# Optimization experiments

Hardware: AMD Instinct MI355X
Metric: run time of the kernel (lower is better)

The kernel has to match this reference:

```python
import jax, jax.numpy as jnp
import numpy as np

# PSLoss constants (from init_kwargs)
MSE_WEIGHT = 0.5
W_CORR = 1.0
W_VAR = 1.0
W_MEAN = 1.0
K = 3           # k_dominant_freqs
MIN_PATCH = 5   # min_patch_len (max(2, 5))
EPS = 1e-8


def setup_inputs() -> dict:
    key = jax.random.key(0)
    k1, k2 = jax.random.split(key)
    B, T, F = 64, 336, 321
    forecast = jax.random.normal(k1, (B, T, F), dtype=jnp.float32)
    target = jax.random.normal(k2, (B, T, F), dtype=jnp.float32)
    return {"forecast": forecast, "target": target}


def _structural_loss(fc, tg):
    """fc, tg: [N, T] flattened (batch*features) series. Returns (total_loss_sum, patch_count)."""
    N, T = tg.shape
    Mmax = T // MIN_PATCH  # max segments per period (period >= MIN_PATCH)

    # --- Fourier adaptive patching (vectorized over all N series) ---
    amp = jnp.abs(jnp.fft.rfft(tg, axis=-1))[:, 1:]           # drop DC, [N, T//2]
    _, rel = jax.lax.top_k(amp, K)                             # [N, K]
    freq_idx = (rel + 1).astype(jnp.float32)
    p = jnp.floor(T / freq_idx).astype(jnp.int32)              # dominant periods [N, K]
    # dedup periods in topk order (the original 'processed_periods' set)
    eq = p[:, :, None] == p[:, None, :]                        # [N, K, K]
    earlier = jnp.tril(jnp.ones((K, K), dtype=bool), -1)       # j < k
    dup = jnp.any(eq & earlier, axis=-1)
    valid_p = (p >= MIN_PATCH) & ~dup                          # [N, K]

    nseg = T // p                                              # [N, K] (p >= 2 always)
    s_idx = jnp.arange(Mmax, dtype=jnp.int32)
    seg_s = p[:, :, None] * s_idx                              # [N, K, Mmax]
    seg_e = seg_s + p[:, :, None]
    seg_v = (s_idx < nseg[:, :, None]) & valid_p[:, :, None]
    rem_s = nseg * p                                           # remaining tail patch
    rem_v = valid_p & ((T - rem_s) >= MIN_PATCH)

    starts = jnp.concatenate([seg_s.reshape(N, -1), rem_s], axis=-1)
    ends = jnp.concatenate([seg_e.reshape(N, -1), jnp.full_like(rem_s, T)], axis=-1)
    valid = jnp.concatenate([seg_v.reshape(N, -1), rem_v], axis=-1)
    # fallback whole-series patch if no patch survived
    none = ~jnp.any(valid, axis=-1, keepdims=True)
    starts = jnp.concatenate([starts, jnp.zeros((N, 1), jnp.int32)], axis=-1)
    ends = jnp.concatenate([ends, jnp.full((N, 1), T, jnp.int32)], axis=-1)
    valid = jnp.concatenate([valid, none], axis=-1)            # [N, M]

    # --- dedup identical (start, end) patches (original list(set(...))) ---
    SENT = (T + 1) * (T + 1)
    keys = jnp.where(valid, starts * (T + 1) + ends, SENT)
    keys = jnp.sort(keys, axis=-1)
    uniq = jnp.concatenate(
        [jnp.ones((N, 1), dtype=bool), keys[:, 1:] != keys[:, :-1]], axis=-1)
    valid = (keys != SENT) & uniq
    s = jnp.where(valid, keys // (T + 1), 0)                   # safe dummy (0,2) when invalid
    e = jnp.where(valid, keys % (T + 1), 2)

    # --- per-patch stats via inclusive prefix sums ---
    def csum(x):
        return jnp.concatenate([jnp.zeros((N, 1), x.dtype), jnp.cumsum(x, axis=-1)], axis=-1)

    cs_t, cs_f = csum(tg), csum(fc)
    cs_tt, cs_ff, cs_tf = csum(tg * tg), csum(fc * fc), csum(tg * fc)

    def seg_sum(cs):
        return jnp.take_along_axis(cs, e, axis=-1) - jnp.take_along_axis(cs, s, axis=-1)

    n = (e - s).astype(jnp.float32)
    St, Sf = seg_sum(cs_t), seg_sum(cs_f)
    Stt, Sff, Stf = seg_sum(cs_tt), seg_sum(cs_ff), seg_sum(cs_tf)
    mt, mf = St / n, Sf / n
    tvs = jnp.maximum(Stt - n * mt * mt, 0.0)   # sum of squared deviations (target)
    fvs = jnp.maximum(Sff - n * mf * mf, 0.0)
    num = Stf - n * mt * mf
    corr = num / (jnp.sqrt(tvs * fvs) + EPS)
    corr_loss = 1.0 - jnp.abs(corr)
    tvar = tvs / (n - 1.0)                      # torch.var is unbiased
    fvar = fvs / (n - 1.0)
    var_loss = jnp.abs(tvar - fvar) / (tvar + EPS)
    mean_loss = jnp.abs(mt - mf) / (jnp.abs(mt) + EPS)
    patch_loss = W_CORR * corr_loss + W_VAR * var_loss + W_MEAN * mean_loss

    total = jnp.sum(jnp.where(valid, patch_loss, 0.0))
    count = jnp.sum(valid)
    return total, count


def reference(forecast, target):
    B, T, F = forecast.shape
    fc = jnp.transpose(forecast, (0, 2, 1)).reshape(B * F, T)
    tg = jnp.transpose(target, (0, 2, 1)).reshape(B * F, T)
    total, count = _structural_loss(fc, tg)
    avg = jnp.where(count > 0,
                    total / jnp.maximum(count, 1).astype(jnp.float32),
                    jnp.float32(0.0))
    mse = jnp.mean((forecast - target) ** 2)
    return MSE_WEIGHT * mse + (1.0 - MSE_WEIGHT) * avg
```

## Files before the change

kernel.cpp:

```cpp
#include <hip/hip_runtime.h>
#include <hip/hip_bf16.h>

#define TT 336
#define NF 321
#define NB 64
#define NSER (NB * NF)
#define WPB 4
#define KP 352
#define LDA 360
#define SPB 16
#define NPATB (NSER / WPB)
#define TSP (TT + 4)

#define SK(b) ((b) + ((b) >> 5))
#define TBL 348

#define TGX 11
#define TGY 11
#define NMSEP (TGX * TGY * NB)

typedef __attribute__((ext_vector_type(8))) short bf16x8;
typedef __attribute__((ext_vector_type(4))) float f32x4;
typedef unsigned long long ULL;

__device__ __forceinline__ unsigned short f2bf(float v) {
    unsigned x = __float_as_uint(v);
    x += 0x7FFFu + ((x >> 16) & 1u);
    return (unsigned short)(x >> 16);
}

__device__ __forceinline__ void ins3(ULL& a0, ULL& a1, ULL& a2, ULL x) {
    ULL hi = a0 > x ? a0 : x;
    ULL lo = a0 > x ? x : a0;
    a0 = hi;
    ULL hi1 = a1 > lo ? a1 : lo;
    ULL lo1 = a1 > lo ? lo : a1;
    a1 = hi1;
    a2 = a2 > lo1 ? a2 : lo1;
}

__global__ void twiddle_k(unsigned short* __restrict__ Wb) {
    int n = blockIdx.x;
    int f = (n >> 1) + 1;
    int isSin = n & 1;
    for (int k = threadIdx.x; k < KP; k += blockDim.x) {
        float v = 0.0f;
        if (k < TT) {
            int r = (f * k) % TT;
            double ang = 6.283185307179586476925286766559 * (double)r / 336.0;
            v = isSin ? (float)sin(ang) : (float)cos(ang);
        }
        Wb[(size_t)n * KP + k] = f2bf(v);
    }
}

__global__ __launch_bounds__(256) void psd_k(const float* __restrict__ tgO,
                                             const unsigned short* __restrict__ Wb,
                                             uint4* __restrict__ topk) {
    __shared__ __align__(16) unsigned short sA[SPB][LDA];
    __shared__ ULL tk3[4][SPB][3];
    const int tid = threadIdx.x;
    const int serBase = blockIdx.x * SPB;

    {
        int f_l = tid & 15, tch = tid >> 4;
        int ser = serBase + f_l;
        int bb = ser / NF, ff = ser - bb * NF;
        const float* base = tgO + (size_t)bb * TT * NF + ff;
        int t0 = tch * 21;
        float v[21];
#pragma unroll
        for (int i = 0; i < 21; i++) v[i] = base[(size_t)(t0 + i) * NF];
#pragma unroll
        for (int i = 0; i < 21; i++) sA[f_l][t0 + i] = f2bf(v[i]);
    }
    if (tid < SPB * 16) sA[tid >> 4][TT + (tid & 15)] = 0;
    __syncthreads();

    const int wave = tid >> 6, lane = tid & 63;
    const int quad = lane >> 4, c = lane & 15;
    const unsigned short* aRow = &sA[c][quad * 8];
    const int ntStart = wave * 5;
    const int ntEnd = (wave == 3) ? 21 : ntStart + 5;

    ULL t0k[4] = {0, 0, 0, 0}, t1k[4] = {0, 0, 0, 0}, t2k[4] = {0, 0, 0, 0};
    for (int nt = ntStart; nt < ntEnd; nt++) {
        const unsigned short* bRow = Wb + (size_t)(nt * 16 + c) * KP + quad * 8;
        f32x4 acc = (f32x4){0.f, 0.f, 0.f, 0.f};
#pragma unroll
        for (int ks = 0; ks < 11; ks++) {
            bf16x8 a = *(const bf16x8*)(aRow + ks * 32);
            bf16x8 b = *(const bf16x8*)(bRow + ks * 32);
            acc = __builtin_amdgcn_mfma_f32_16x16x32_bf16(a, b, acc, 0, 0, 0);
        }
        int n = nt * 16 + c;
        unsigned fidx = (unsigned)((n >> 1) + 1);
        unsigned ftag = 0xFFFFFFFFu - fidx;
        bool odd = (n & 1) != 0;
#pragma unroll
        for (int r = 0; r < 4; r++) {
            float v = acc[r];
            float p = v * v;
            p += __shfl_xor(p, 1, 64);
            ULL key = odd ? 0ull
                          : (((ULL)__float_as_uint(p) << 32) | (ULL)ftag);
            ins3(t0k[r], t1k[r], t2k[r], key);
        }
    }
#pragma unroll
    for (int m = 2; m <= 8; m <<= 1) {
#pragma unroll
        for (int r = 0; r < 4; r++) {
            ULL b0 = __shfl_xor(t0k[r], m, 64);
            ULL b1 = __shfl_xor(t1k[r], m, 64);
            ULL b2 = __shfl_xor(t2k[r], m, 64);
            ins3(t0k[r], t1k[r], t2k[r], b0);
            ins3(t0k[r], t1k[r], t2k[r], b1);
            ins3(t0k[r], t1k[r], t2k[r], b2);
        }
    }
    if (c == 0) {
#pragma unroll
        for (int r = 0; r < 4; r++) {
            int s = quad * 4 + r;
            tk3[wave][s][0] = t0k[r];
            tk3[wave][s][1] = t1k[r];
            tk3[wave][s][2] = t2k[r];
        }
    }
    __syncthreads();
    if (tid < SPB) {
        ULL k0 = 0, k1 = 0, k2 = 0;
#pragma unroll
        for (int wv = 0; wv < 4; wv++) {
#pragma unroll
            for (int j = 0; j < 3; j++) ins3(k0, k1, k2, tk3[wv][tid][j]);
        }
        unsigned f0 = 0xFFFFFFFFu - (unsigned)(k0 & 0xFFFFFFFFull);
        unsigned f1 = 0xFFFFFFFFu - (unsigned)(k1 & 0xFFFFFFFFull);
        unsigned f2 = 0xFFFFFFFFu - (unsigned)(k2 & 0xFFFFFFFFull);
        topk[serBase + tid] = make_uint4(f0, f1, f2, 0u);
    }
}

__global__ __launch_bounds__(256) void transpose_k(const float* __restrict__ fc,
                                                   const float* __restrict__ tg,
                                                   float2* __restrict__ out,
                                                   double* __restrict__ msep,
                                                   double* __restrict__ acc) {
    __shared__ float ta[32][33];
    __shared__ float tb[32][33];
    __shared__ double wacc[4];
    const int b = blockIdx.z;
    const int t0 = blockIdx.x * 32, f0 = blockIdx.y * 32;
    const int tx = threadIdx.x, ty = threadIdx.y;
    const size_t base = (size_t)b * TT * NF;
    double ms = 0.0;
#pragma unroll
    for (int k = 0; k < 4; k++) {
        int t = t0 + ty + 8 * k, f = f0 + tx;
        if (t < TT && f < NF) {
            float a = tg[base + (size_t)t * NF + f];
            float c = fc[base + (size_t)t * NF + f];
            ta[ty + 8 * k][tx] = a;
            tb[ty + 8 * k][tx] = c;
            double d = (double)a - (double)c;
            ms += d * d;
        }
    }
    __syncthreads();
#pragma unroll
    for (int k = 0; k < 4; k++) {
        int f = f0 + ty + 8 * k, t = t0 + tx;
        if (t < TT && f < NF) {
            out[((size_t)b * NF + f) * TT + t] =
                make_float2(ta[tx][ty + 8 * k], tb[tx][ty + 8 * k]);
        }
    }
    for (int off = 32; off; off >>= 1) ms += __shfl_down(ms, off, 64);
    int flat = ty * 32 + tx;
    int lane = flat & 63, wid = flat >> 6;
    if (lane == 0) wacc[wid] = ms;
    __syncthreads();
    if (flat == 0) {
        double tot = wacc[0] + wacc[1] + wacc[2] + wacc[3];
        if (msep) {
            int blk = (blockIdx.z * TGY + blockIdx.y) * TGX + blockIdx.x;
            msep[blk] = tot;
        } else {
            atomicAdd(&acc[0], tot);
        }
    }
}

__global__ void mse_k(const float* __restrict__ fc, const float* __restrict__ tg,
                      double* __restrict__ acc) {
    const size_t N4 = (size_t)NB * TT * NF / 4;
    const float4* a4 = (const float4*)fc;
    const float4* b4 = (const float4*)tg;
    double s = 0.0;
    for (size_t i = (size_t)blockIdx.x * blockDim.x + threadIdx.x; i < N4;
         i += (size_t)gridDim.x * blockDim.x) {
        float4 a = a4[i], b = b4[i];
        double d0 = (double)a.x - (double)b.x;
        double d1 = (double)a.y - (double)b.y;
        double d2 = (double)a.z - (double)b.z;
        double d3 = (double)a.w - (double)b.w;
        s += d0 * d0 + d1 * d1 + d2 * d2 + d3 * d3;
    }
    for (int off = 32; off; off >>= 1) s += __shfl_down(s, off, 64);
    __shared__ double wsum[4];
    int flat = threadIdx.x;
    int lane = flat & 63, wid = flat >> 6;
    if (lane == 0) wsum[wid] = s;
    __syncthreads();
    if (flat == 0) atomicAdd(&acc[0], wsum[0] + wsum[1] + wsum[2] + wsum[3]);
}

__device__ __forceinline__ double patch_loss(double S1, double S2, double S3,
                                             double S4, double S5, double nn) {
    double mt = S1 / nn, mf = S2 / nn;
    double tvs = S3 - nn * mt * mt; tvs = tvs > 0.0 ? tvs : 0.0;
    double fvs = S4 - nn * mf * mf; fvs = fvs > 0.0 ? fvs : 0.0;
    double num = S5 - nn * mt * mf;
    double corr = num / (sqrt(tvs * fvs) + 1e-8);
    double closs = 1.0 - fabs(corr);
    double tvar = tvs / (nn - 1.0), fvar = fvs / (nn - 1.0);
    double vloss = fabs(tvar - fvar) / (tvar + 1e-8);
    double mloss = fabs(mt - mf) / (fabs(mt) + 1e-8);
    return closs + vloss + mloss;
}

__device__ __forceinline__ double patch_loss_fast(double S1, double S2,
                                                  float S3, float S4, float S5,
                                                  int n) {
    float nnf = (float)n;
    float invf = 1.0f / nnf;
    float s1f = (float)S1, s2f = (float)S2;
    float tvs = S3 - s1f * s1f * invf; tvs = tvs > 0.f ? tvs : 0.f;
    float fvs = S4 - s2f * s2f * invf; fvs = fvs > 0.f ? fvs : 0.f;
    float num = S5 - s1f * s2f * invf;
    float corr = num / (sqrtf(tvs * fvs) + 1e-8f);
    float closs = 1.0f - fabsf(corr);
    float vloss = fabsf(tvs - fvs) / (tvs + (nnf - 1.0f) * 1e-8f);
    double mloss = fabs(S1 - S2) / (fabs(S1) + (double)n * 1e-8);
    return (double)(closs + vloss) + mloss;
}

struct PatchCfg {
    int P[3], nseg[3], rs[3];
    bool vp[3], hr[3];
};

__device__ __forceinline__ void make_cfg(int fr0, int fr1, int fr2, PatchCfg& c) {
    c.P[0] = TT / fr0; c.P[1] = TT / fr1; c.P[2] = TT / fr2;
    c.vp[0] = (c.P[0] >= 5);
    c.vp[1] = (c.P[1] >= 5) && (c.P[1] != c.P[0]);
    c.vp[2] = (c.P[2] >= 5) && (c.P[2] != c.P[0]) && (c.P[2] != c.P[1]);
#pragma unroll
    for (int q = 0; q < 3; q++) {
        c.nseg[q] = TT / c.P[q];
        c.rs[q] = c.nseg[q] * c.P[q];
        c.hr[q] = c.vp[q] && ((TT - c.rs[q]) >= 5);
    }
}

__device__ __forceinline__ bool slot_patch(const PatchCfg& c, int i, int& s, int& e) {
    bool kept = false;
    s = 0; e = 0;
    if (i < 204) {
        int k = (i >= 136) ? 2 : ((i >= 68) ? 1 : 0);
        int si = i - k * 68;
        if (c.vp[k]) {
            if (si < c.nseg[k]) { s = c.P[k] * si; e = s + c.P[k]; kept = true; }
            else if (si == c.nseg[k] && c.hr[k]) { s = c.rs[k]; e = TT; kept = true; }
            if (kept) {
#pragma unroll
                for (int j = 0; j < 2; j++) {
                    if (j < k && c.vp[j]) {
                        bool dup = (s == c.rs[j]) && (e == TT) && c.hr[j];
                        int len = e - s;
                        if (len == c.P[j] && s < c.rs[j] && (s % c.P[j]) == 0) dup = true;
                        if (dup) kept = false;
                    }
                }
            }
        }
    }
    return kept;
}

__global__ __launch_bounds__(256) void patch_k(const float* __restrict__ fcO,
                                               const float* __restrict__ tgO,
                                               const uint4* __restrict__ topk,
                                               double2* __restrict__ pairs,
                                               double* __restrict__ msep) {
    __shared__ __align__(16) char smem[2 * WPB * TBL * 8 + 3 * WPB * TBL * 4];
    double (*d1)[TBL] = (double(*)[TBL])smem;
    double (*d2)[TBL] = (double(*)[TBL])(smem + WPB * TBL * 8);
    char* regB = smem + 2 * WPB * TBL * 8;
    float2* tsB = (float2*)regB;
    float (*t3)[TBL] = (float(*)[TBL])regB;
    float (*t4)[TBL] = (float(*)[TBL])(regB + WPB * TBL * 4);
    float (*t5)[TBL] = (float(*)[TBL])(regB + 2 * WPB * TBL * 4);
    __shared__ double wms[WPB];

    const int tid = threadIdx.x;
    const int w = tid >> 6, lane = tid & 63;
    const int lb = (blockIdx.x & 7) * (NPATB / 8) + (blockIdx.x >> 3);
    const int ser = lb * WPB + w;

    {
        const int j = tid & 3;
        const int serj = lb * WPB + j;
        const int bb = serj / NF, ff = serj - bb * NF;
        const float* tb_ = tgO + (size_t)bb * TT * NF + ff;
        const float* fb_ = fcO + (size_t)bb * TT * NF + ff;
        const int tb0 = tid >> 2;
        float2* row = tsB + j * TSP;
        double ms = 0.0;
#pragma unroll
        for (int i = 0; i < 6; i++) {
            int t = tb0 + 64 * i;
            if (t < TT) {
                float a = tb_[(size_t)t * NF];
                float c = fb_[(size_t)t * NF];
                row[t] = make_float2(a, c);
                double d = (double)a - (double)c;
                ms += d * d;
            }
        }
        for (int off = 32; off; off >>= 1) ms += __shfl_down(ms, off, 64);
        if (lane == 0) wms[w] = ms;
    }
    __syncthreads();
    if (tid == 0) msep[lb] = wms[0] + wms[1] + wms[2] + wms[3];

    float2 loc[6];
    double c1 = 0, c2 = 0;
    float c3 = 0, c4 = 0, c5 = 0;
    if (lane < 56) {
        const float4* lp = (const float4*)(tsB + w * TSP + 6 * lane);
        float4 va = lp[0], vb = lp[1], vc = lp[2];
        loc[0] = make_float2(va.x, va.y); loc[1] = make_float2(va.z, va.w);
        loc[2] = make_float2(vb.x, vb.y); loc[3] = make_float2(vb.z, vb.w);
        loc[4] = make_float2(vc.x, vc.y); loc[5] = make_float2(vc.z, vc.w);
#pragma unroll
        for (int i = 0; i < 6; i++) {
            float a = loc[i].x, b = loc[i].y;
            c1 += (double)a; c2 += (double)b;
            c3 = fmaf(a, a, c3); c4 = fmaf(b, b, c4); c5 = fmaf(a, b, c5);
        }
    }

    double s1 = c1, s2 = c2;
    float s3 = c3, s4 = c4, s5 = c5;
#pragma unroll
    for (int off = 1; off < 64; off <<= 1) {
        double y1 = __shfl_up(s1, off, 64);
        double y2 = __shfl_up(s2, off, 64);
        float y3 = __shfl_up(s3, off, 64);
        float y4 = __shfl_up(s4, off, 64);
        float y5 = __shfl_up(s5, off, 64);
        if (lane >= off) { s1 += y1; s2 += y2; s3 += y3; s4 += y4; s5 += y5; }
    }

    __syncthreads();

    if (lane == 63) {
        d1[w][SK(0)] = 0.0; d2[w][SK(0)] = 0.0;
        t3[w][SK(0)] = 0.f; t4[w][SK(0)] = 0.f; t5[w][SK(0)] = 0.f;
    }
    if (lane < 56) {
        double r1 = s1 - c1, r2 = s2 - c2;
        float r3 = s3 - c3, r4 = s4 - c4, r5 = s5 - c5;
#pragma unroll
        for (int i = 0; i < 6; i++) {
            float a = loc[i].x, b = loc[i].y;
            r1 += (double)a; r2 += (double)b;
            r3 = fmaf(a, a, r3); r4 = fmaf(b, b, r4); r5 = fmaf(a, b, r5);
            int ix = SK(6 * lane + i + 1);
            d1[w][ix] = r1; d2[w][ix] = r2;
            t3[w][ix] = r3; t4[w][ix] = r4; t5[w][ix] = r5;
        }
    }
    __syncthreads();

    uint4 tk = topk[ser];
    PatchCfg cfg;
    make_cfg((int)tk.x, (int)tk.y, (int)tk.z, cfg);

    double lsum = 0.0, lcnt = 0.0;
    ULL anyMask = 0ull;
#pragma unroll
    for (int rI = 0; rI < 4; rI++) {
        int s, e;
        bool kept = slot_patch(cfg, lane + 64 * rI, s, e);
        ULL bal = __ballot(kept);
        anyMask |= bal;
        if (bal == 0ull) continue;
        if (kept) {
            int is = SK(s), ie = SK(e);
            double S1 = d1[w][ie] - d1[w][is];
            double S2 = d2[w][ie] - d2[w][is];
            float S3 = t3[w][ie] - t3[w][is];
            float S4 = t4[w][ie] - t4[w][is];
            float S5 = t5[w][ie] - t5[w][is];
            lsum += patch_loss_fast(S1, S2, S3, S4, S5, e - s);
            lcnt += 1.0;
        }
    }

    if (anyMask == 0ull) {
        if (lane == 0) {
            int ie = SK(TT);
            lsum += patch_loss_fast(d1[w][ie], d2[w][ie], t3[w][ie],
                                    t4[w][ie], t5[w][ie], TT);
            lcnt += 1.0;
        }
    }

    for (int off = 32; off; off >>= 1) {
        lsum += __shfl_down(lsum, off, 64);
        lcnt += __shfl_down(lcnt, off, 64);
    }
    if (lane == 0) pairs[ser] = make_double2(lsum, lcnt);
}

__device__ __forceinline__ void patch_body(const float2* tsw, int lane,
                                           int fr0, int fr1, int fr2,
                                           double& lsum, double& lcnt) {
    PatchCfg cfg;
    make_cfg(fr0, fr1, fr2, cfg);
    ULL anyMask = 0ull;
#pragma unroll
    for (int rI = 0; rI < 4; rI++) {
        int s, e;
        bool kept = slot_patch(cfg, lane + 64 * rI, s, e);
        anyMask |= __ballot(kept);
        if (kept) {
            double S1 = 0, S2 = 0, S3 = 0, S4 = 0, S5 = 0;
            for (int t = s; t < e; t++) {
                float2 v = tsw[t];
                double a = (double)v.x, b = (double)v.y;
                S1 += a; S2 += b;
                S3 += a * a; S4 += b * b; S5 += a * b;
            }
            lsum += patch_loss(S1, S2, S3, S4, S5, (double)(e - s));
            lcnt += 1.0;
        }
    }
    if (anyMask == 0ull) {
        double S1 = 0, S2 = 0, S3 = 0, S4 = 0, S5 = 0;
        for (int t = lane; t < TT; t += 64) {
            float2 v = tsw[t];
            double a = (double)v.x, b = (double)v.y;
            S1 += a; S2 += b;
            S3 += a * a; S4 += b * b; S5 += a * b;
        }
        for (int off = 32; off; off >>= 1) {
            S1 += __shfl_down(S1, off, 64);
            S2 += __shfl_down(S2, off, 64);
            S3 += __shfl_down(S3, off, 64);
            S4 += __shfl_down(S4, off, 64);
            S5 += __shfl_down(S5, off, 64);
        }
        if (lane == 0) {
            lsum += patch_loss(S1, S2, S3, S4, S5, (double)TT);
            lcnt += 1.0;
        }
    }
}

__global__ __launch_bounds__(256, 6) void series_k(const float2* __restrict__ tsG,
                                                   const float* __restrict__ fcG,
                                                   const float* __restrict__ tgG,
                                                   int transposed,
                                                   double2* __restrict__ pairs,
                                                   double* __restrict__ acc) {
    const int w = threadIdx.x >> 6, lane = threadIdx.x & 63;
    const int ser = blockIdx.x * WPB + w;
    __shared__ float2 ts[WPB][TT];
    __shared__ float4 zb[WPB][84];

    if (transposed) {
        const float2* sp = tsG + (size_t)ser * TT;
        for (int t = lane; t < TT; t += 64) ts[w][t] = sp[t];
    } else {
        int b = ser / NF, f = ser - b * NF;
        const float* tp = tgG + (size_t)b * TT * NF + f;
        const float* fp = fcG + (size_t)b * TT * NF + f;
        for (int t = lane; t < TT; t += 64)
            ts[w][t] = make_float2(tp[(size_t)t * NF], fp[(size_t)t * NF]);
    }
    __syncthreads();

    for (int t = lane; t < 84; t += 64) {
        float x0 = ts[w][t].x, x1 = ts[w][t + 84].x;
        float x2 = ts[w][t + 168].x, x3 = ts[w][t + 252].x;
        float a = x0 + x2, b2 = x1 + x3, c = x0 - x2, d = x1 - x3;
        zb[w][t] = make_float4(a + b2, a - b2, c, d);
    }
    __syncthreads();

    const double TWOPI = 6.283185307179586476925286766559;
    int fb[3] = {1 + lane, 65 + lane, 129 + lane};
    float cc[3], sn[3], re[3], im[3], cd[3], sd[3], sgn[3];
    int selA[3];
#pragma unroll
    for (int q = 0; q < 3; q++) {
        int f = fb[q], cls = f & 3;
        double dl = (double)f * (TWOPI / 336.0);
        cd[q] = (float)cos(dl);
        sd[q] = (float)sin(dl);
        cc[q] = 1.0f; sn[q] = 0.0f; re[q] = 0.0f; im[q] = 0.0f;
        sgn[q] = (cls == 1) ? -1.0f : ((cls == 3) ? 1.0f : 0.0f);
        selA[q] = (cls == 0) ? 0 : ((cls == 2) ? 1 : 2);
    }
    for (int t = 0; t < 84; t++) {
        float4 zv = zb[w][t];
#pragma unroll
        for (int q = 0; q < 3; q++) {
            float zr = (selA[q] == 0) ? zv.x : ((selA[q] == 1) ? zv.y : zv.z);
            float zi = sgn[q] * zv.w;
            re[q] = fmaf(zr, cc[q], re[q]);
            re[q] = fmaf(zi, sn[q], re[q]);
            im[q] = fmaf(zi, cc[q], im[q]);
            im[q] = fmaf(-zr, sn[q], im[q]);
            float nc = fmaf(cc[q], cd[q], -(sn[q] * sd[q]));
            float ns = fmaf(sn[q], cd[q], cc[q] * sd[q]);
            cc[q] = nc; sn[q] = ns;
        }
    }

    ULL k0 = 0, k1 = 0, k2 = 0;
#pragma unroll
    for (int q = 0; q < 3; q++) {
        float a2 = fmaf(re[q], re[q], im[q] * im[q]);
        ULL key = ((ULL)__float_as_uint(a2) << 32) |
                  (ULL)(0xFFFFFFFFu - (unsigned)fb[q]);
        if (fb[q] > 168) key = 0ull;
        ins3(k0, k1, k2, key);
    }
    for (int m = 1; m < 64; m <<= 1) {
        ULL b0 = __shfl_xor(k0, m, 64);
        ULL b1 = __shfl_xor(k1, m, 64);
        ULL b2 = __shfl_xor(k2, m, 64);
        ins3(k0, k1, k2, b0); ins3(k0, k1, k2, b1); ins3(k0, k1, k2, b2);
    }

    int fr0 = (int)(0xFFFFFFFFu - (unsigned)(k0 & 0xFFFFFFFFull));
    int fr1 = (int)(0xFFFFFFFFu - (unsigned)(k1 & 0xFFFFFFFFull));
    int fr2 = (int)(0xFFFFFFFFu - (unsigned)(k2 & 0xFFFFFFFFull));

    double lsum = 0.0, lcnt = 0.0;
    patch_body(&ts[w][0], lane, fr0, fr1, fr2, lsum, lcnt);

    for (int off = 32; off; off >>= 1) {
        lsum += __shfl_down(lsum, off, 64);
        lcnt += __shfl_down(lcnt, off, 64);
    }
    if (lane == 0) {
        if (pairs) {
            pairs[ser] = make_double2(lsum, lcnt);
        } else {
            atomicAdd(&acc[1], lsum);
            atomicAdd(&acc[2], lcnt);
        }
    }
}

__global__ __launch_bounds__(1024) void reduce_k(const double2* __restrict__ pairs,
                                                 const double* __restrict__ msep,
                                                 int nmse,
                                                 float* __restrict__ out) {
    const int tid = threadIdx.x;
    double ls = 0.0, lc = 0.0, ms = 0.0;
    for (int i = tid; i < NSER; i += 1024) {
        double2 p = pairs[i];
        ls += p.x; lc += p.y;
    }
    for (int i = tid; i < nmse; i += 1024) ms += msep[i];
    for (int off = 32; off; off >>= 1) {
        ls += __shfl_down(ls, off, 64);
        lc += __shfl_down(lc, off, 64);
        ms += __shfl_down(ms, off, 64);
    }
    __shared__ double sl[16], sc[16], sm[16];
    int lane = tid & 63, wid = tid >> 6;
    if (lane == 0) { sl[wid] = ls; sc[wid] = lc; sm[wid] = ms; }
    __syncthreads();
    if (tid == 0) {
        double L = 0, C = 0, M = 0;
        for (int i = 0; i < 16; i++) { L += sl[i]; C += sc[i]; M += sm[i]; }
        double mse = M / (double)((size_t)NB * TT * NF);
        double avg = (C > 0.0) ? (L / C) : 0.0;
        out[0] = (float)(0.5 * mse + 0.5 * avg);
    }
}

__global__ void finalize_k(const double* __restrict__ acc, float* __restrict__ out) {
    double mse = acc[0] / (double)((size_t)NB * TT * NF);
    double avg = (acc[2] > 0.0) ? (acc[1] / acc[2]) : 0.0;
    out[0] = (float)(0.5 * mse + 0.5 * avg);
}

extern "C" void kernel_launch(void* const* d_in, const int* in_sizes, int n_in,
                              void* d_out, int out_size, void* d_ws, size_t ws_size,
                              hipStream_t stream) {
    const float* fc = (const float*)d_in[0];
    const float* tg = (const float*)d_in[1];
    float* out = (float*)d_out;
    char* ws = (char*)d_ws;
    double* acc = (double*)ws;

    const size_t OFF_MSE = 64;
    const size_t OFF_PAIR = OFF_MSE + (size_t)NMSEP * sizeof(double);
    const size_t OFF_TOP = OFF_PAIR + (size_t)NSER * sizeof(double2);
    const size_t OFF_W = OFF_TOP + (size_t)NSER * sizeof(uint4);
    const size_t OFF_END2 = OFF_W + (size_t)TT * KP * sizeof(unsigned short);
    const size_t bytesT = (size_t)NSER * TT * sizeof(float2);
    const bool big2 = (ws_size >= OFF_END2);
    const size_t R3_OFF_TS = OFF_PAIR + (size_t)NSER * sizeof(double2);
    const bool big = !big2 && (ws_size >= R3_OFF_TS + bytesT);
    const bool mid = !big2 && !big && (ws_size >= OFF_MSE + bytesT);

    double* msep = (double*)(ws + OFF_MSE);
    double2* pairs = (double2*)(ws + OFF_PAIR);
    uint4* topkBuf = (uint4*)(ws + OFF_TOP);
    unsigned short* Wb = (unsigned short*)(ws + OFF_W);

    dim3 tg_grid(TGX, TGY, NB);
    dim3 tg_blk(32, 8);

    if (big2) {
        twiddle_k<<<TT, 128, 0, stream>>>(Wb);
        psd_k<<<NSER / SPB, 256, 0, stream>>>(tg, Wb, topkBuf);
        patch_k<<<NPATB, 64 * WPB, 0, stream>>>(fc, tg, topkBuf, pairs, msep);
        reduce_k<<<1, 1024, 0, stream>>>(pairs, msep, NPATB, out);
    } else if (big) {
        float2* tsT = (float2*)(ws + R3_OFF_TS);
        transpose_k<<<tg_grid, tg_blk, 0, stream>>>(fc, tg, tsT, msep, acc);
        series_k<<<NSER / WPB, 64 * WPB, 0, stream>>>(tsT, fc, tg, 1, pairs, acc);
        reduce_k<<<1, 1024, 0, stream>>>(pairs, msep, NMSEP, out);
    } else if (mid) {
        float2* tsT = (float2*)(ws + OFF_MSE);
        hipMemsetAsync(d_ws, 0, 64, stream);
        transpose_k<<<tg_grid, tg_blk, 0, stream>>>(fc, tg, tsT, nullptr, acc);
        series_k<<<NSER / WPB, 64 * WPB, 0, stream>>>(tsT, fc, tg, 1, nullptr, acc);
        finalize_k<<<1, 1, 0, stream>>>(acc, out);
    } else {
        hipMemsetAsync(d_ws, 0, 64, stream);
        mse_k<<<1024, 256, 0, stream>>>(fc, tg, acc);
        series_k<<<NSER / WPB, 64 * WPB, 0, stream>>>(nullptr, fc, tg, 0, nullptr, acc);
        finalize_k<<<1, 1, 0, stream>>>(acc, out);
    }
}
```

Baseline: 170.5 us.

## Split PSD frequency tiles across four blocks per series group and merge top-k

```diff
diff --git a/kernel.cpp b/kernel.cpp
--- a/kernel.cpp
+++ b/kernel.cpp
@@ -9,6 +9,8 @@
 #define KP 352
 #define LDA 360
 #define SPB 16
+#define NTG 4
+#define NPSB ((NSER / SPB) * NTG)
 #define NPATB (NSER / WPB)
 #define TSP (TT + 4)
 
@@ -56,11 +58,13 @@
 
 __global__ __launch_bounds__(256) void psd_k(const float* __restrict__ tgO,
                                              const unsigned short* __restrict__ Wb,
-                                             uint4* __restrict__ topk) {
+                                             ULL* __restrict__ cand) {
     __shared__ __align__(16) unsigned short sA[SPB][LDA];
     __shared__ ULL tk3[4][SPB][3];
     const int tid = threadIdx.x;
-    const int serBase = blockIdx.x * SPB;
+    const int lb = (blockIdx.x & 7) * (NPSB / 8) + (blockIdx.x >> 3);
+    const int serBlk = lb >> 2, g = lb & 3;
+    const int serBase = serBlk * SPB;
 
     {
         int f_l = tid & 15, tch = tid >> 4;
@@ -80,11 +84,11 @@
     const int wave = tid >> 6, lane = tid & 63;
     const int quad = lane >> 4, c = lane & 15;
     const unsigned short* aRow = &sA[c][quad * 8];
-    const int ntStart = wave * 5;
-    const int ntEnd = (wave == 3) ? 21 : ntStart + 5;
+    const int ntStart = g * 5 + wave;
+    const int ntEnd = (g == 3) ? 21 : g * 5 + 5;
 
     ULL t0k[4] = {0, 0, 0, 0}, t1k[4] = {0, 0, 0, 0}, t2k[4] = {0, 0, 0, 0};
-    for (int nt = ntStart; nt < ntEnd; nt++) {
+    for (int nt = ntStart; nt < ntEnd; nt += 4) {
         const unsigned short* bRow = Wb + (size_t)(nt * 16 + c) * KP + quad * 8;
         f32x4 acc = (f32x4){0.f, 0.f, 0.f, 0.f};
 #pragma unroll
@@ -136,11 +140,23 @@
 #pragma unroll
             for (int j = 0; j < 3; j++) ins3(k0, k1, k2, tk3[wv][tid][j]);
         }
-        unsigned f0 = 0xFFFFFFFFu - (unsigned)(k0 & 0xFFFFFFFFull);
-        unsigned f1 = 0xFFFFFFFFu - (unsigned)(k1 & 0xFFFFFFFFull);
-        unsigned f2 = 0xFFFFFFFFu - (unsigned)(k2 & 0xFFFFFFFFull);
-        topk[serBase + tid] = make_uint4(f0, f1, f2, 0u);
-    }
+        ULL* cp = cand + ((size_t)(serBase + tid) * NTG + g) * 3;
+        cp[0] = k0; cp[1] = k1; cp[2] = k2;
+    }
+}
+
+__global__ __launch_bounds__(256) void topkmerge_k(const ULL* __restrict__ cand,
+                                                   uint4* __restrict__ topk) {
+    int ser = blockIdx.x * 256 + threadIdx.x;
+    if (ser >= NSER) return;
+    const ULL* cp = cand + (size_t)ser * NTG * 3;
+    ULL k0 = 0, k1 = 0, k2 = 0;
+#pragma unroll
+    for (int j = 0; j < NTG * 3; j++) ins3(k0, k1, k2, cp[j]);
+    unsigned f0 = 0xFFFFFFFFu - (unsigned)(k0 & 0xFFFFFFFFull);
+    unsigned f1 = 0xFFFFFFFFu - (unsigned)(k1 & 0xFFFFFFFFull);
+    unsigned f2 = 0xFFFFFFFFu - (unsigned)(k2 & 0xFFFFFFFFull);
+    topk[ser] = make_uint4(f0, f1, f2, 0u);
 }
 
 __global__ __launch_bounds__(256) void transpose_k(const float* __restrict__ fc,
@@ -618,7 +634,8 @@
     const size_t OFF_PAIR = OFF_MSE + (size_t)NMSEP * sizeof(double);
     const size_t OFF_TOP = OFF_PAIR + (size_t)NSER * sizeof(double2);
     const size_t OFF_W = OFF_TOP + (size_t)NSER * sizeof(uint4);
-    const size_t OFF_END2 = OFF_W + (size_t)TT * KP * sizeof(unsigned short);
+    const size_t OFF_CAND = OFF_W + (size_t)TT * KP * sizeof(unsigned short);
+    const size_t OFF_END2 = OFF_CAND + (size_t)NSER * NTG * 3 * sizeof(ULL);
     const size_t bytesT = (size_t)NSER * TT * sizeof(float2);
     const bool big2 = (ws_size >= OFF_END2);
     const size_t R3_OFF_TS = OFF_PAIR + (size_t)NSER * sizeof(double2);
@@ -629,13 +646,15 @@
     double2* pairs = (double2*)(ws + OFF_PAIR);
     uint4* topkBuf = (uint4*)(ws + OFF_TOP);
     unsigned short* Wb = (unsigned short*)(ws + OFF_W);
+    ULL* cand = (ULL*)(ws + OFF_CAND);
 
     dim3 tg_grid(TGX, TGY, NB);
     dim3 tg_blk(32, 8);
 
     if (big2) {
         twiddle_k<<<TT, 128, 0, stream>>>(Wb);
-        psd_k<<<NSER / SPB, 256, 0, stream>>>(tg, Wb, topkBuf);
+        psd_k<<<NPSB, 256, 0, stream>>>(tg, Wb, cand);
+        topkmerge_k<<<(NSER + 255) / 256, 256, 0, stream>>>(cand, topkBuf);
         patch_k<<<NPATB, 64 * WPB, 0, stream>>>(fc, tg, topkBuf, pairs, msep);
         reduce_k<<<1, 1024, 0, stream>>>(pairs, msep, NPATB, out);
     } else if (big) {
```

New measurement: 191.4 us. 1.12x slower.
